# Optimization experiments

Hardware: AMD Instinct MI355X
Metric: run time of the kernel (lower is better)

The kernel has to match this reference:

```python
import jax, jax.numpy as jnp
import numpy as np

NUM_HEADS = 4
D_MODEL = 256
HEAD_DIM = D_MODEL // NUM_HEADS  # 64
B, N = 8, 2048


def _proj(x, W, b):
    # Conv1d with kernel_size=1 == pointwise linear over channel dim
    # x: [B, C_in, N], W: [C_out, C_in], b: [C_out]
    return jnp.einsum('oi,bin->bon', W, x) + b[None, :, None]


def setup_inputs() -> dict:
    key = jax.random.key(0)
    ks = jax.random.split(key, 11)
    s = 1.0 / np.sqrt(D_MODEL)
    return {
        'query': jax.random.normal(ks[0], (B, D_MODEL, N), jnp.float32),
        'key':   jax.random.normal(ks[1], (B, D_MODEL, N), jnp.float32),
        'value': jax.random.normal(ks[2], (B, D_MODEL, N), jnp.float32),
        'Wq': jax.random.normal(ks[3], (D_MODEL, D_MODEL), jnp.float32) * s,
        'bq': jax.random.normal(ks[4], (D_MODEL,), jnp.float32) * 0.01,
        'Wk': jax.random.normal(ks[5], (D_MODEL, D_MODEL), jnp.float32) * s,
        'bk': jax.random.normal(ks[6], (D_MODEL,), jnp.float32) * 0.01,
        'Wv': jax.random.normal(ks[7], (D_MODEL, D_MODEL), jnp.float32) * s,
        'bv': jax.random.normal(ks[8], (D_MODEL,), jnp.float32) * 0.01,
        'Wm': jax.random.normal(ks[9], (D_MODEL, D_MODEL), jnp.float32) * s,
        'bm': jax.random.normal(ks[10], (D_MODEL,), jnp.float32) * 0.01,
    }


def reference(query, key, value, Wq, bq, Wk, bk, Wv, bv, Wm, bm):
    b = query.shape[0]
    # project then split channels into (head_dim, num_heads): [B, d, h, N]
    q = _proj(query, Wq, bq).reshape(b, HEAD_DIM, NUM_HEADS, -1)
    k = _proj(key,   Wk, bk).reshape(b, HEAD_DIM, NUM_HEADS, -1)
    v = _proj(value, Wv, bv).reshape(b, HEAD_DIM, NUM_HEADS, -1)
    scale = 1.0 / jnp.sqrt(jnp.asarray(HEAD_DIM, q.dtype))
    scores = jnp.einsum('bdhn,bdhm->bhnm', q, k) * scale  # [B,H,N,N]
    prob = jax.nn.softmax(scores, axis=-1)
    x = jnp.einsum('bhnm,bdhm->bdhn', prob, v)  # [B,d,H,N]
    x = x.reshape(b, HEAD_DIM * NUM_HEADS, -1)  # [B, d_model, N]
    return _proj(x, Wm, bm)
```

## Files before the change

kernel.cpp:

```cpp
#include <hip/hip_runtime.h>
#include <math.h>


constexpr int BATCH  = 8;
constexpr int DMODEL = 256;
constexpr int SEQ    = 2048;
constexpr int HDIM   = 64;
constexpr int TM     = 64;
constexpr int NJT    = SEQ / TM;

typedef _Float16 half2_t __attribute__((ext_vector_type(2)));
typedef _Float16 half4_t __attribute__((ext_vector_type(4)));
typedef _Float16 half8_t __attribute__((ext_vector_type(8)));
typedef float    float4_t __attribute__((ext_vector_type(4)));

static __device__ __forceinline__ void ld16_lds(const void* g, void* l) {
    __builtin_amdgcn_global_load_lds(
        (const __attribute__((address_space(1))) unsigned*)g,
        (__attribute__((address_space(3))) unsigned*)l, 16, 0, 0);
}

static __device__ __forceinline__ half8_t cvt8(const float4 w0, const float4 w1) {
    half8_t a;
    a[0] = (_Float16)w0.x; a[1] = (_Float16)w0.y;
    a[2] = (_Float16)w0.z; a[3] = (_Float16)w0.w;
    a[4] = (_Float16)w1.x; a[5] = (_Float16)w1.y;
    a[6] = (_Float16)w1.z; a[7] = (_Float16)w1.w;
    return a;
}

__global__ __launch_bounds__(256, 3)
void gemm_qkv(const float* __restrict__ Wq, const float* __restrict__ Wk,
              const float* __restrict__ Wv, const float* __restrict__ Wm,
              const float* __restrict__ bq, const float* __restrict__ bk,
              const float* __restrict__ bv,
              const float* __restrict__ Xq, const float* __restrict__ Xk,
              const float* __restrict__ Xv, _Float16* __restrict__ qT,
              _Float16* __restrict__ kT, _Float16* __restrict__ vT,
              _Float16* __restrict__ wfp)
{
    if (blockIdx.y == 24) {
        const int r = blockIdx.x * 8 + (threadIdx.x >> 5);
        const int c32 = threadIdx.x & 31;
        half8_t o8;
        #pragma unroll
        for (int e = 0; e < 8; ++e) {
            const int hd = c32 * 8 + e;
            o8[e] = (_Float16)Wm[r * DMODEL + 4 * (hd & 63) + (hd >> 6)];
        }
        *(half8_t*)&wfp[(size_t)r * DMODEL + c32 * 8] = o8;
        return;
    }

    const int n0 = blockIdx.x * 64;
    const int proj = blockIdx.y >> 3, b = blockIdx.y & 7;
    const float* W    = proj == 0 ? Wq : proj == 1 ? Wk : Wv;
    const float* bias = proj == 0 ? bq : proj == 1 ? bk : bv;
    const float* X    = (proj == 0 ? Xq : proj == 1 ? Xk : Xv)
                        + (size_t)b * DMODEL * SEQ;
    const float qs = (proj == 0) ? 0.18033688011112042f : 1.0f;

    __shared__ __align__(16) char lds[50432];
    float*    T  = (float*)lds;
    _Float16* Xs = (_Float16*)(lds + 16640);
    _Float16* Tw = (_Float16*)lds;

    const int tid = threadIdx.x, tn = tid & 15, tc = tid >> 4;

    #pragma unroll
    for (int cc = 0; cc < 4; ++cc) {
        __syncthreads();
        #pragma unroll
        for (int i = 0; i < 4; ++i) {
            const int c = tc + 16 * i;
            const float4 v = *(const float4*)&X[(size_t)(cc * 64 + c) * SEQ + n0 + tn * 4];
            T[c * 65 + tn * 4 + 0] = v.x; T[c * 65 + tn * 4 + 1] = v.y;
            T[c * 65 + tn * 4 + 2] = v.z; T[c * 65 + tn * 4 + 3] = v.w;
        }
        __syncthreads();
        #pragma unroll
        for (int i = 0; i < 4; ++i) {
            const int n = tc + 16 * i;
            half4_t h4;
            #pragma unroll
            for (int j = 0; j < 4; ++j) h4[j] = (_Float16)T[(tn * 4 + j) * 65 + n];
            *(half4_t*)&Xs[n * 264 + cc * 64 + tn * 4] = h4;
        }
    }
    __syncthreads();

    const int w = tid >> 6, lane = tid & 63;
    const int lm = lane & 15, g = lane >> 4, g8 = g * 8;
    const int cw0 = w * 64;

    float4_t acc[4][4];
    #pragma unroll
    for (int mt = 0; mt < 4; ++mt)
        #pragma unroll
        for (int nt = 0; nt < 4; ++nt) acc[mt][nt] = (float4_t){0.f, 0.f, 0.f, 0.f};

    #pragma unroll
    for (int k0 = 0; k0 < DMODEL; k0 += 64) {
        half8_t a[4][2], bb[4][2];
        #pragma unroll
        for (int mt = 0; mt < 4; ++mt)
            #pragma unroll
            for (int kd = 0; kd < 2; ++kd) {
                const float* wp = &W[(size_t)(cw0 + mt * 16 + lm) * DMODEL
                                     + k0 + kd * 32 + g8];
                a[mt][kd] = cvt8(*(const float4*)wp, *(const float4*)(wp + 4));
            }
        #pragma unroll
        for (int nt = 0; nt < 4; ++nt)
            #pragma unroll
            for (int kd = 0; kd < 2; ++kd)
                bb[nt][kd] = *(const half8_t*)&Xs[(nt * 16 + lm) * 264
                                                  + k0 + kd * 32 + g8];
        #pragma unroll
        for (int kd = 0; kd < 2; ++kd)
            #pragma unroll
            for (int mt = 0; mt < 4; ++mt)
                #pragma unroll
                for (int nt = 0; nt < 4; ++nt)
                    acc[mt][nt] = __builtin_amdgcn_mfma_f32_16x16x32_f16(
                        a[mt][kd], bb[nt][kd], acc[mt][nt], 0, 0, 0);
    }
    __syncthreads();

    #pragma unroll
    for (int mt = 0; mt < 4; ++mt) {
        const float4 b4 = *(const float4*)&bias[cw0 + mt * 16 + g * 4];
        const float bb4[4] = {b4.x, b4.y, b4.z, b4.w};
        #pragma unroll
        for (int nt = 0; nt < 4; ++nt) {
            half4_t pk;
            #pragma unroll
            for (int r = 0; r < 4; ++r)
                pk[r] = (_Float16)((acc[mt][nt][r] + bb4[r]) * qs);
            *(half4_t*)&Tw[((w * 64 + nt * 16 + lm)) * 68 + mt * 16 + g * 4] = pk;
        }
    }
    __syncthreads();

    if (proj < 2) {
        _Float16* dst = (proj == 0 ? qT : kT);
        const int h = w;
        const int dcg = lane & 7, nlb = lane >> 3;
        #pragma unroll
        for (int it = 0; it < 8; ++it) {
            const int nl = it * 8 + nlb;
            const int hs = (nl & 3) | (((nl >> 3) & 1) << 2);
            half8_t ch;
            #pragma unroll
            for (int e = 0; e < 8; ++e) {
                ch[e] = Tw[((dcg >> 1) * 64 + nl) * 68
                           + 4 * ((dcg & 1) * 8 + e) + h];
            }
            const int chunk = dcg ^ hs;
            *(half8_t*)&dst[((size_t)(b * 4 + h) * SEQ + n0 + nl) * HDIM
                            + chunk * 8] = ch;
        }
    } else {
        const int h = w;
        const int jc = lane & 7, db = lane >> 3;
        const size_t tilebase =
            (((size_t)(b * 4 + h) * NJT + (n0 >> 6)) * HDIM) * (size_t)TM;
        #pragma unroll
        for (int it = 0; it < 8; ++it) {
            const int d = it * 8 + db;
            half8_t ch;
            #pragma unroll
            for (int e = 0; e < 8; ++e) {
                ch[e] = Tw[((d >> 4) * 64 + jc * 8 + e) * 68
                           + 4 * (d & 15) + h];
            }
            *(half8_t*)&vT[tilebase + (size_t)d * TM + ((jc ^ (d & 7)) << 3)] = ch;
        }
    }
}

__global__ __launch_bounds__(256, 2)
void attn_f16(const _Float16* __restrict__ qT, const _Float16* __restrict__ kT,
              const _Float16* __restrict__ vT, _Float16* __restrict__ xp)
{
    const int lid = blockIdx.x;
    const int work = (lid & 7) * 64 + (lid >> 3);
    const int bh = work >> 4, b = bh >> 2, h = bh & 3;
    const int ib = work & 15;
    const int tid = threadIdx.x, wid = tid >> 6, lane = tid & 63;
    const int lm = lane & 15, g = lane >> 4;
    const int i0 = ib * 128 + wid * 32;

    __shared__ _Float16 Kb[2][TM * HDIM];
    __shared__ _Float16 Vb[2][TM * HDIM];

    const int hq = (lm & 3) | (((lm >> 3) & 1) << 2);
    const int hk = (lm & 3) | (((lm >> 2) & 1) << 2);
    const int rbase = 8 * (lm >> 2) + (lm & 3);

    half8_t bq[2][2];
    const _Float16* qbase = qT + (size_t)bh * SEQ * HDIM;
    #pragma unroll
    for (int rt = 0; rt < 2; ++rt)
        #pragma unroll
        for (int kd = 0; kd < 2; ++kd) {
            const int row = i0 + rt * 16 + lm;
            bq[rt][kd] = *(const half8_t*)(qbase + (size_t)row * HDIM
                                           + (((kd * 4 + g) ^ hq) << 3));
        }

    const char* kt = (const char*)(kT + (size_t)bh * SEQ * HDIM);
    const char* vt = (const char*)(vT + (size_t)bh * NJT * TM * HDIM);

    float4_t o[2][4];
    float rsum[2][2] = {{0.f, 0.f}, {0.f, 0.f}};
    #pragma unroll
    for (int rt = 0; rt < 2; ++rt)
        #pragma unroll
        for (int dt = 0; dt < 4; ++dt) o[rt][dt] = (float4_t){0.f, 0.f, 0.f, 0.f};

    #define STAGE(jt, bu)                                                     \
        {                                                                     \
            const char* kg = kt + (size_t)(jt) * 8192;                        \
            const char* vg = vt + (size_t)(jt) * 8192;                        \
            _Pragma("unroll")                                                 \
            for (int p = 0; p < 2; ++p) {                                     \
                const int c = wid + p * 4;                                    \
                ld16_lds(kg + c * 1024 + lane * 16, (char*)&Kb[bu][0] + c * 1024); \
                ld16_lds(vg + c * 1024 + lane * 16, (char*)&Vb[bu][0] + c * 1024); \
            }                                                                 \
        }

    STAGE(0, 0);
    __syncthreads();

    for (int jt = 0; jt < NJT; ++jt) {
        const int cur = jt & 1;
        if (jt + 1 < NJT) STAGE(jt + 1, cur ^ 1);

        float4_t s[2][2][2];
        #pragma unroll
        for (int jb = 0; jb < 2; ++jb)
            #pragma unroll
            for (int u = 0; u < 2; ++u)
                #pragma unroll
                for (int rt = 0; rt < 2; ++rt)
                    s[jb][u][rt] = (float4_t){0.f, 0.f, 0.f, 0.f};
        #pragma unroll
        for (int kd = 0; kd < 2; ++kd)
            #pragma unroll
            for (int jb = 0; jb < 2; ++jb)
                #pragma unroll
                for (int u = 0; u < 2; ++u) {
                    const int jrow = jb * 32 + rbase + 4 * u;
                    const half8_t fk = *(const half8_t*)
                        &Kb[cur][jrow * HDIM + (((kd * 4 + g) ^ hk) << 3)];
                    #pragma unroll
                    for (int rt = 0; rt < 2; ++rt)
                        s[jb][u][rt] = __builtin_amdgcn_mfma_f32_16x16x32_f16(
                            fk, bq[rt][kd], s[jb][u][rt], 0, 0, 0);
                }

        half8_t ap[2][2];
        #pragma unroll
        for (int jb = 0; jb < 2; ++jb)
            #pragma unroll
            for (int rt = 0; rt < 2; ++rt) {
                half8_t p;
                #pragma unroll
                for (int r = 0; r < 4; ++r) {
                    const float e0 = __builtin_amdgcn_exp2f(s[jb][0][rt][r]);
                    const float e1 = __builtin_amdgcn_exp2f(s[jb][1][rt][r]);
                    rsum[jb][rt] += e0;
                    rsum[jb][rt] += e1;
                    p[r]     = (_Float16)e0;
                    p[r + 4] = (_Float16)e1;
                }
                ap[jb][rt] = p;
            }

        #pragma unroll
        for (int jb = 0; jb < 2; ++jb)
            #pragma unroll
            for (int dt = 0; dt < 4; ++dt) {
                const int d = dt * 16 + lm;
                const half8_t fv = *(const half8_t*)
                    &Vb[cur][d * TM + (((jb * 4 + g) ^ (lm & 7)) << 3)];
                #pragma unroll
                for (int rt = 0; rt < 2; ++rt)
                    o[rt][dt] = __builtin_amdgcn_mfma_f32_16x16x32_f16(
                        ap[jb][rt], fv, o[rt][dt], 0, 0, 0);
            }
        __syncthreads();
    }

    #pragma unroll
    for (int rt = 0; rt < 2; ++rt) {
        float v = rsum[0][rt] + rsum[1][rt];
        v += __shfl_xor(v, 16);
        v += __shfl_xor(v, 32);
        float inv[4];
        #pragma unroll
        for (int r = 0; r < 4; ++r)
            inv[r] = 1.0f / __shfl(v, 4 * g + r);
        #pragma unroll
        for (int dt = 0; dt < 4; ++dt) {
            const int d = dt * 16 + lm;
            #pragma unroll
            for (int r = 0; r < 4; ++r) {
                const int n = i0 + rt * 16 + 4 * g + r;
                xp[((size_t)b * SEQ + n) * DMODEL + h * HDIM + d] =
                    (_Float16)(o[rt][dt][r] * inv[r]);
            }
        }
    }
    #undef STAGE
}

__global__ __launch_bounds__(256, 3)
void gemm_final(const _Float16* __restrict__ wfp, const float* __restrict__ bias,
                const _Float16* __restrict__ xp, float* __restrict__ out)
{
    const int n0 = blockIdx.x * 32, b = blockIdx.y;
    const int tid = threadIdx.x, w = tid >> 6, lane = tid & 63;
    const int lm = lane & 15, g = lane >> 4, g8 = g * 8;
    const int cw0 = w * 64;

    __shared__ _Float16 Xc[32 * DMODEL];

    {
        const int c8 = tid & 31, nb = tid >> 5;
        const _Float16* P = xp + ((size_t)b * SEQ + n0) * DMODEL;
        #pragma unroll
        for (int j = 0; j < 4; ++j) {
            const int n = nb * 4 + j;
            const half8_t v = *(const half8_t*)&P[(size_t)n * DMODEL + c8 * 8];
            *(half8_t*)&Xc[n * DMODEL + ((c8 ^ (n & 7)) << 3)] = v;
        }
    }
    __syncthreads();

    float4_t acc[4][2];
    #pragma unroll
    for (int mt = 0; mt < 4; ++mt)
        #pragma unroll
        for (int nt = 0; nt < 2; ++nt) acc[mt][nt] = (float4_t){0.f, 0.f, 0.f, 0.f};

    #pragma unroll
    for (int k0 = 0; k0 < DMODEL; k0 += 64) {
        half8_t a[4][2], bb[2][2];
        #pragma unroll
        for (int mt = 0; mt < 4; ++mt)
            #pragma unroll
            for (int kd = 0; kd < 2; ++kd)
                a[mt][kd] = *(const half8_t*)&wfp[(size_t)(cw0 + mt * 16 + lm) * DMODEL
                                                  + k0 + kd * 32 + g8];
        #pragma unroll
        for (int nt = 0; nt < 2; ++nt)
            #pragma unroll
            for (int kd = 0; kd < 2; ++kd) {
                const int n = nt * 16 + lm;
                const int c8 = (k0 >> 3) + kd * 4 + g;
                bb[nt][kd] = *(const half8_t*)
                    &Xc[n * DMODEL + ((c8 ^ (n & 7)) << 3)];
            }
        #pragma unroll
        for (int kd = 0; kd < 2; ++kd)
            #pragma unroll
            for (int mt = 0; mt < 4; ++mt)
                #pragma unroll
                for (int nt = 0; nt < 2; ++nt)
                    acc[mt][nt] = __builtin_amdgcn_mfma_f32_16x16x32_f16(
                        a[mt][kd], bb[nt][kd], acc[mt][nt], 0, 0, 0);
    }

    #pragma unroll
    for (int mt = 0; mt < 4; ++mt)
        #pragma unroll
        for (int r = 0; r < 4; ++r) {
            const int co = cw0 + mt * 16 + g * 4 + r;
            const float bv_ = bias[co];
            #pragma unroll
            for (int nt = 0; nt < 2; ++nt)
                out[((size_t)b * DMODEL + co) * SEQ + n0 + nt * 16 + lm] =
                    acc[mt][nt][r] + bv_;
        }
}

extern "C" void kernel_launch(void* const* d_in, const int* in_sizes, int n_in,
                              void* d_out, int out_size, void* d_ws, size_t ws_size,
                              hipStream_t stream) {
    const float* query = (const float*)d_in[0];
    const float* key_  = (const float*)d_in[1];
    const float* value = (const float*)d_in[2];
    const float* Wq = (const float*)d_in[3];  const float* bq = (const float*)d_in[4];
    const float* Wk = (const float*)d_in[5];  const float* bk = (const float*)d_in[6];
    const float* Wv = (const float*)d_in[7];  const float* bv = (const float*)d_in[8];
    const float* Wm = (const float*)d_in[9];  const float* bm = (const float*)d_in[10];
    float* out = (float*)d_out;

    const size_t bufElems = (size_t)BATCH * DMODEL * SEQ;
    _Float16* qT = (_Float16*)d_ws;
    _Float16* kT = qT + bufElems;
    _Float16* vT = kT + bufElems;
    _Float16* xp = vT + bufElems;
    _Float16* wfp = xp + bufElems;

    gemm_qkv<<<dim3(SEQ / 64, 25), 256, 0, stream>>>(
        Wq, Wk, Wv, Wm, bq, bk, bv, query, key_, value, qT, kT, vT, wfp);
    attn_f16<<<dim3(512), 256, 0, stream>>>(qT, kT, vT, xp);
    gemm_final<<<dim3(SEQ / 32, BATCH), 256, 0, stream>>>(
        wfp, bm, xp, out);
}
```

Baseline: 178.6 us.

## Use 8 waves per attention block and split output GEMM over channel halves

The attention kernel goes from 4 waves handling 32 query rows each to 8 waves handling 16 rows each per 128-row block. Each wave now keeps half the accumulators, and the K/V staging is split across 8 waves with one load per wave. The final projection GEMM gains a grid dimension that splits the 256 output channels into two halves, doubling block count with smaller per-wave tiles and a higher occupancy hint. The aim is better latency hiding and more parallelism, at the cost of each K/V LDS tile being reused by fewer MFMAs per wave, and of the final GEMM reloading the X tile twice.

```diff
diff --git a/kernel.cpp b/kernel.cpp
--- a/kernel.cpp
+++ b/kernel.cpp
@@ -179,7 +179,7 @@
     }
 }
 
-__global__ __launch_bounds__(256, 2)
+__global__ __launch_bounds__(512, 2)
 void attn_f16(const _Float16* __restrict__ qT, const _Float16* __restrict__ kT,
               const _Float16* __restrict__ vT, _Float16* __restrict__ xp)
 {
@@ -189,7 +189,7 @@
     const int ib = work & 15;
     const int tid = threadIdx.x, wid = tid >> 6, lane = tid & 63;
     const int lm = lane & 15, g = lane >> 4;
-    const int i0 = ib * 128 + wid * 32;
+    const int i0 = ib * 128 + wid * 16;
 
     __shared__ _Float16 Kb[2][TM * HDIM];
     __shared__ _Float16 Vb[2][TM * HDIM];
@@ -198,37 +198,29 @@
     const int hk = (lm & 3) | (((lm >> 2) & 1) << 2);
     const int rbase = 8 * (lm >> 2) + (lm & 3);
 
-    half8_t bq[2][2];
+    half8_t bq[2];
     const _Float16* qbase = qT + (size_t)bh * SEQ * HDIM;
     #pragma unroll
-    for (int rt = 0; rt < 2; ++rt)
-        #pragma unroll
-        for (int kd = 0; kd < 2; ++kd) {
-            const int row = i0 + rt * 16 + lm;
-            bq[rt][kd] = *(const half8_t*)(qbase + (size_t)row * HDIM
-                                           + (((kd * 4 + g) ^ hq) << 3));
-        }
+    for (int kd = 0; kd < 2; ++kd) {
+        const int row = i0 + lm;
+        bq[kd] = *(const half8_t*)(qbase + (size_t)row * HDIM
+                                   + (((kd * 4 + g) ^ hq) << 3));
+    }
 
     const char* kt = (const char*)(kT + (size_t)bh * SEQ * HDIM);
     const char* vt = (const char*)(vT + (size_t)bh * NJT * TM * HDIM);
 
-    float4_t o[2][4];
-    float rsum[2][2] = {{0.f, 0.f}, {0.f, 0.f}};
-    #pragma unroll
-    for (int rt = 0; rt < 2; ++rt)
-        #pragma unroll
-        for (int dt = 0; dt < 4; ++dt) o[rt][dt] = (float4_t){0.f, 0.f, 0.f, 0.f};
+    float4_t o[4];
+    float rsum[2] = {0.f, 0.f};
+    #pragma unroll
+    for (int dt = 0; dt < 4; ++dt) o[dt] = (float4_t){0.f, 0.f, 0.f, 0.f};
 
     #define STAGE(jt, bu)                                                     \
         {                                                                     \
             const char* kg = kt + (size_t)(jt) * 8192;                        \
             const char* vg = vt + (size_t)(jt) * 8192;                        \
-            _Pragma("unroll")                                                 \
-            for (int p = 0; p < 2; ++p) {                                     \
-                const int c = wid + p * 4;                                    \
-                ld16_lds(kg + c * 1024 + lane * 16, (char*)&Kb[bu][0] + c * 1024); \
-                ld16_lds(vg + c * 1024 + lane * 16, (char*)&Vb[bu][0] + c * 1024); \
-            }                                                                 \
+            ld16_lds(kg + wid * 1024 + lane * 16, (char*)&Kb[bu][0] + wid * 1024); \
+            ld16_lds(vg + wid * 1024 + lane * 16, (char*)&Vb[bu][0] + wid * 1024); \
         }
 
     STAGE(0, 0);
@@ -238,14 +230,12 @@
         const int cur = jt & 1;
         if (jt + 1 < NJT) STAGE(jt + 1, cur ^ 1);
 
-        float4_t s[2][2][2];
+        float4_t s[2][2];
         #pragma unroll
         for (int jb = 0; jb < 2; ++jb)
             #pragma unroll
             for (int u = 0; u < 2; ++u)
-                #pragma unroll
-                for (int rt = 0; rt < 2; ++rt)
-                    s[jb][u][rt] = (float4_t){0.f, 0.f, 0.f, 0.f};
+                s[jb][u] = (float4_t){0.f, 0.f, 0.f, 0.f};
         #pragma unroll
         for (int kd = 0; kd < 2; ++kd)
             #pragma unroll
@@ -255,29 +245,25 @@
                     const int jrow = jb * 32 + rbase + 4 * u;
                     const half8_t fk = *(const half8_t*)
                         &Kb[cur][jrow * HDIM + (((kd * 4 + g) ^ hk) << 3)];
-                    #pragma unroll
-                    for (int rt = 0; rt < 2; ++rt)
-                        s[jb][u][rt] = __builtin_amdgcn_mfma_f32_16x16x32_f16(
-                            fk, bq[rt][kd], s[jb][u][rt], 0, 0, 0);
+                    s[jb][u] = __builtin_amdgcn_mfma_f32_16x16x32_f16(
+                        fk, bq[kd], s[jb][u], 0, 0, 0);
                 }
 
-        half8_t ap[2][2];
-        #pragma unroll
-        for (int jb = 0; jb < 2; ++jb)
-            #pragma unroll
-            for (int rt = 0; rt < 2; ++rt) {
-                half8_t p;
-                #pragma unroll
-                for (int r = 0; r < 4; ++r) {
-                    const float e0 = __builtin_amdgcn_exp2f(s[jb][0][rt][r]);
-                    const float e1 = __builtin_amdgcn_exp2f(s[jb][1][rt][r]);
-                    rsum[jb][rt] += e0;
-                    rsum[jb][rt] += e1;
-                    p[r]     = (_Float16)e0;
-                    p[r + 4] = (_Float16)e1;
-                }
-                ap[jb][rt] = p;
-            }
+        half8_t ap[2];
+        #pragma unroll
+        for (int jb = 0; jb < 2; ++jb) {
+            half8_t p;
+            #pragma unroll
+            for (int r = 0; r < 4; ++r) {
+                const float e0 = __builtin_amdgcn_exp2f(s[jb][0][r]);
+                const float e1 = __builtin_amdgcn_exp2f(s[jb][1][r]);
+                rsum[jb] += e0;
+                rsum[jb] += e1;
+                p[r]     = (_Float16)e0;
+                p[r + 4] = (_Float16)e1;
+            }
+            ap[jb] = p;
+        }
 
         #pragma unroll
         for (int jb = 0; jb < 2; ++jb)
@@ -286,17 +272,14 @@
                 const int d = dt * 16 + lm;
                 const half8_t fv = *(const half8_t*)
                     &Vb[cur][d * TM + (((jb * 4 + g) ^ (lm & 7)) << 3)];
-                #pragma unroll
-                for (int rt = 0; rt < 2; ++rt)
-                    o[rt][dt] = __builtin_amdgcn_mfma_f32_16x16x32_f16(
-                        ap[jb][rt], fv, o[rt][dt], 0, 0, 0);
+                o[dt] = __builtin_amdgcn_mfma_f32_16x16x32_f16(
+                    ap[jb], fv, o[dt], 0, 0, 0);
             }
         __syncthreads();
     }
 
-    #pragma unroll
-    for (int rt = 0; rt < 2; ++rt) {
-        float v = rsum[0][rt] + rsum[1][rt];
+    {
+        float v = rsum[0] + rsum[1];
         v += __shfl_xor(v, 16);
         v += __shfl_xor(v, 32);
         float inv[4];
@@ -308,23 +291,23 @@
             const int d = dt * 16 + lm;
             #pragma unroll
             for (int r = 0; r < 4; ++r) {
-                const int n = i0 + rt * 16 + 4 * g + r;
+                const int n = i0 + 4 * g + r;
                 xp[((size_t)b * SEQ + n) * DMODEL + h * HDIM + d] =
-                    (_Float16)(o[rt][dt][r] * inv[r]);
+                    (_Float16)(o[dt][r] * inv[r]);
             }
         }
     }
     #undef STAGE
 }
 
-__global__ __launch_bounds__(256, 3)
+__global__ __launch_bounds__(256, 4)
 void gemm_final(const _Float16* __restrict__ wfp, const float* __restrict__ bias,
                 const _Float16* __restrict__ xp, float* __restrict__ out)
 {
-    const int n0 = blockIdx.x * 32, b = blockIdx.y;
+    const int n0 = blockIdx.x * 32, m0 = blockIdx.y * 128, b = blockIdx.z;
     const int tid = threadIdx.x, w = tid >> 6, lane = tid & 63;
     const int lm = lane & 15, g = lane >> 4, g8 = g * 8;
-    const int cw0 = w * 64;
+    const int cw0 = m0 + w * 32;
 
     __shared__ _Float16 Xc[32 * DMODEL];
 
@@ -340,17 +323,17 @@
     }
     __syncthreads();
 
-    float4_t acc[4][2];
-    #pragma unroll
-    for (int mt = 0; mt < 4; ++mt)
+    float4_t acc[2][2];
+    #pragma unroll
+    for (int mt = 0; mt < 2; ++mt)
         #pragma unroll
         for (int nt = 0; nt < 2; ++nt) acc[mt][nt] = (float4_t){0.f, 0.f, 0.f, 0.f};
 
     #pragma unroll
     for (int k0 = 0; k0 < DMODEL; k0 += 64) {
-        half8_t a[4][2], bb[2][2];
-        #pragma unroll
-        for (int mt = 0; mt < 4; ++mt)
+        half8_t a[2][2], bb[2][2];
+        #pragma unroll
+        for (int mt = 0; mt < 2; ++mt)
             #pragma unroll
             for (int kd = 0; kd < 2; ++kd)
                 a[mt][kd] = *(const half8_t*)&wfp[(size_t)(cw0 + mt * 16 + lm) * DMODEL
@@ -367,7 +350,7 @@
         #pragma unroll
         for (int kd = 0; kd < 2; ++kd)
             #pragma unroll
-            for (int mt = 0; mt < 4; ++mt)
+            for (int mt = 0; mt < 2; ++mt)
                 #pragma unroll
                 for (int nt = 0; nt < 2; ++nt)
                     acc[mt][nt] = __builtin_amdgcn_mfma_f32_16x16x32_f16(
@@ -375,7 +358,7 @@
     }
 
     #pragma unroll
-    for (int mt = 0; mt < 4; ++mt)
+    for (int mt = 0; mt < 2; ++mt)
         #pragma unroll
         for (int r = 0; r < 4; ++r) {
             const int co = cw0 + mt * 16 + g * 4 + r;
@@ -408,7 +391,7 @@
 
     gemm_qkv<<<dim3(SEQ / 64, 25), 256, 0, stream>>>(
         Wq, Wk, Wv, Wm, bq, bk, bv, query, key_, value, qT, kT, vT, wfp);
-    attn_f16<<<dim3(512), 256, 0, stream>>>(qT, kT, vT, xp);
-    gemm_final<<<dim3(SEQ / 32, BATCH), 256, 0, stream>>>(
+    attn_f16<<<dim3(512), 512, 0, stream>>>(qT, kT, vT, xp);
+    gemm_final<<<dim3(SEQ / 32, 2, BATCH), 256, 0, stream>>>(
         wfp, bm, xp, out);
 }
```

New measurement: 180.9 us. Within noise of the previous version (+1.3%).

## Interleave QK, softmax and PV with sched barriers; split final GEMM over channels

Applied to the files above, without the earlier changes.

The attention inner loop is restructured so the QK product, exp and PV product run per 32-row half. Explicit sched_group_barrier directives interleave LDS reads, MFMAs and VALU exp work, and s_setprio raises wave priority during compute. The aim is to overlap exp/VALU latency with matrix-core work. Separately, the final projection GEMM is split across two output-channel halves per block, giving more blocks and higher occupancy (launch bounds 4). The cost is that the Xc tile is loaded once per half, so LDS staging is done twice. The hand-written schedule may also be fragile, and the PV macro parameter uses a non-ASCII identifier.

```diff
diff --git a/kernel.cpp b/kernel.cpp
--- a/kernel.cpp
+++ b/kernel.cpp
@@ -231,6 +231,50 @@
             }                                                                 \
         }
 
+    #define QK(jb, sdst)                                                      \
+        _Pragma("unroll")                                                     \
+        for (int kd = 0; kd < 2; ++kd)                                        \
+            _Pragma("unroll")                                                 \
+            for (int u = 0; u < 2; ++u) {                                     \
+                const int jrow = (jb) * 32 + rbase + 4 * u;                   \
+                const half8_t fk = *(const half8_t*)                          \
+                    &Kb[cur][jrow * HDIM + (((kd * 4 + g) ^ hk) << 3)];       \
+                _Pragma("unroll")                                             \
+                for (int rt = 0; rt < 2; ++rt)                                \
+                    sdst[u][rt] = __builtin_amdgcn_mfma_f32_16x16x32_f16(     \
+                        fk, bq[rt][kd], sdst[u][rt], 0, 0, 0);                \
+            }
+
+    #define EXPP(jb, ssrc, apd)                                               \
+        _Pragma("unroll")                                                     \
+        for (int rt = 0; rt < 2; ++rt) {                                      \
+            half8_t p;                                                        \
+            _Pragma("unroll")                                                 \
+            for (int r = 0; r < 4; ++r) {                                     \
+                const float e0 = __builtin_amdgcn_exp2f(ssrc[0][rt][r]);      \
+                const float e1 = __builtin_amdgcn_exp2f(ssrc[1][rt][r]);      \
+                rsum[jb][rt] += e0;                                           \
+                rsum[jb][rt] += e1;                                           \
+                p[r]     = (_Float16)e0;                                      \
+                p[r + 4] = (_Float16)e1;                                      \
+            }                                                                 \
+            apd[rt] = p;                                                      \
+        }
+
+    #define PV(jb, apس)                                                       \
+        _Pragma("unroll")                                                     \
+        for (int dt = 0; dt < 4; ++dt) {                                      \
+            const int d = dt * 16 + lm;                                       \
+            const half8_t fv = *(const half8_t*)                              \
+                &Vb[cur][d * TM + ((((jb) * 4 + g) ^ (lm & 7)) << 3)];        \
+            _Pragma("unroll")                                                 \
+            for (int rt = 0; rt < 2; ++rt)                                    \
+                o[rt][dt] = __builtin_amdgcn_mfma_f32_16x16x32_f16(           \
+                    apس[rt], fv, o[rt][dt], 0, 0, 0);                         \
+        }
+
+    #define SGB(m, n) __builtin_amdgcn_sched_group_barrier((m), (n), 0)
+
     STAGE(0, 0);
     __syncthreads();
 
@@ -238,59 +282,38 @@
         const int cur = jt & 1;
         if (jt + 1 < NJT) STAGE(jt + 1, cur ^ 1);
 
-        float4_t s[2][2][2];
-        #pragma unroll
-        for (int jb = 0; jb < 2; ++jb)
-            #pragma unroll
-            for (int u = 0; u < 2; ++u)
-                #pragma unroll
-                for (int rt = 0; rt < 2; ++rt)
-                    s[jb][u][rt] = (float4_t){0.f, 0.f, 0.f, 0.f};
-        #pragma unroll
-        for (int kd = 0; kd < 2; ++kd)
-            #pragma unroll
-            for (int jb = 0; jb < 2; ++jb)
-                #pragma unroll
-                for (int u = 0; u < 2; ++u) {
-                    const int jrow = jb * 32 + rbase + 4 * u;
-                    const half8_t fk = *(const half8_t*)
-                        &Kb[cur][jrow * HDIM + (((kd * 4 + g) ^ hk) << 3)];
-                    #pragma unroll
-                    for (int rt = 0; rt < 2; ++rt)
-                        s[jb][u][rt] = __builtin_amdgcn_mfma_f32_16x16x32_f16(
-                            fk, bq[rt][kd], s[jb][u][rt], 0, 0, 0);
-                }
-
-        half8_t ap[2][2];
-        #pragma unroll
-        for (int jb = 0; jb < 2; ++jb)
+        __builtin_amdgcn_s_setprio(1);
+
+        float4_t s0[2][2], s1[2][2];
+        #pragma unroll
+        for (int u = 0; u < 2; ++u)
             #pragma unroll
             for (int rt = 0; rt < 2; ++rt) {
-                half8_t p;
-                #pragma unroll
-                for (int r = 0; r < 4; ++r) {
-                    const float e0 = __builtin_amdgcn_exp2f(s[jb][0][rt][r]);
-                    const float e1 = __builtin_amdgcn_exp2f(s[jb][1][rt][r]);
-                    rsum[jb][rt] += e0;
-                    rsum[jb][rt] += e1;
-                    p[r]     = (_Float16)e0;
-                    p[r + 4] = (_Float16)e1;
-                }
-                ap[jb][rt] = p;
-            }
-
-        #pragma unroll
-        for (int jb = 0; jb < 2; ++jb)
-            #pragma unroll
-            for (int dt = 0; dt < 4; ++dt) {
-                const int d = dt * 16 + lm;
-                const half8_t fv = *(const half8_t*)
-                    &Vb[cur][d * TM + (((jb * 4 + g) ^ (lm & 7)) << 3)];
-                #pragma unroll
-                for (int rt = 0; rt < 2; ++rt)
-                    o[rt][dt] = __builtin_amdgcn_mfma_f32_16x16x32_f16(
-                        ap[jb][rt], fv, o[rt][dt], 0, 0, 0);
-            }
+                s0[u][rt] = (float4_t){0.f, 0.f, 0.f, 0.f};
+                s1[u][rt] = (float4_t){0.f, 0.f, 0.f, 0.f};
+            }
+
+        half8_t ap0[2], ap1[2];
+        QK(0, s0);
+        QK(1, s1);
+        EXPP(0, s0, ap0);
+        PV(0, ap0);
+        EXPP(1, s1, ap1);
+        PV(1, ap1);
+
+        SGB(0x20, 4);
+        SGB(0x100, 4); SGB(0x8, 8);
+        #pragma unroll
+        for (int i = 0; i < 4; ++i) {
+            SGB(0x100, 1); SGB(0x8, 2); SGB(0x2, 12);
+        }
+        #pragma unroll
+        for (int i = 0; i < 4; ++i) {
+            SGB(0x100, 1); SGB(0x8, 2); SGB(0x2, 12);
+        }
+        SGB(0x100, 4); SGB(0x8, 8);
+
+        __builtin_amdgcn_s_setprio(0);
         __syncthreads();
     }
 
@@ -315,16 +338,20 @@
         }
     }
     #undef STAGE
-}
-
-__global__ __launch_bounds__(256, 3)
+    #undef QK
+    #undef EXPP
+    #undef PV
+    #undef SGB
+}
+
+__global__ __launch_bounds__(256, 4)
 void gemm_final(const _Float16* __restrict__ wfp, const float* __restrict__ bias,
                 const _Float16* __restrict__ xp, float* __restrict__ out)
 {
-    const int n0 = blockIdx.x * 32, b = blockIdx.y;
+    const int n0 = blockIdx.x * 32, m0 = blockIdx.y * 128, b = blockIdx.z;
     const int tid = threadIdx.x, w = tid >> 6, lane = tid & 63;
     const int lm = lane & 15, g = lane >> 4, g8 = g * 8;
-    const int cw0 = w * 64;
+    const int cw0 = m0 + w * 32;
 
     __shared__ _Float16 Xc[32 * DMODEL];
 
@@ -340,17 +367,17 @@
     }
     __syncthreads();
 
-    float4_t acc[4][2];
-    #pragma unroll
-    for (int mt = 0; mt < 4; ++mt)
+    float4_t acc[2][2];
+    #pragma unroll
+    for (int mt = 0; mt < 2; ++mt)
         #pragma unroll
         for (int nt = 0; nt < 2; ++nt) acc[mt][nt] = (float4_t){0.f, 0.f, 0.f, 0.f};
 
     #pragma unroll
     for (int k0 = 0; k0 < DMODEL; k0 += 64) {
-        half8_t a[4][2], bb[2][2];
-        #pragma unroll
-        for (int mt = 0; mt < 4; ++mt)
+        half8_t a[2][2], bb[2][2];
+        #pragma unroll
+        for (int mt = 0; mt < 2; ++mt)
             #pragma unroll
             for (int kd = 0; kd < 2; ++kd)
                 a[mt][kd] = *(const half8_t*)&wfp[(size_t)(cw0 + mt * 16 + lm) * DMODEL
@@ -367,7 +394,7 @@
         #pragma unroll
         for (int kd = 0; kd < 2; ++kd)
             #pragma unroll
-            for (int mt = 0; mt < 4; ++mt)
+            for (int mt = 0; mt < 2; ++mt)
                 #pragma unroll
                 for (int nt = 0; nt < 2; ++nt)
                     acc[mt][nt] = __builtin_amdgcn_mfma_f32_16x16x32_f16(
@@ -375,7 +402,7 @@
     }
 
     #pragma unroll
-    for (int mt = 0; mt < 4; ++mt)
+    for (int mt = 0; mt < 2; ++mt)
         #pragma unroll
         for (int r = 0; r < 4; ++r) {
             const int co = cw0 + mt * 16 + g * 4 + r;
@@ -409,6 +436,6 @@
     gemm_qkv<<<dim3(SEQ / 64, 25), 256, 0, stream>>>(
         Wq, Wk, Wv, Wm, bq, bk, bv, query, key_, value, qT, kT, vT, wfp);
     attn_f16<<<dim3(512), 256, 0, stream>>>(qT, kT, vT, xp);
-    gemm_final<<<dim3(SEQ / 32, BATCH), 256, 0, stream>>>(
+    gemm_final<<<dim3(SEQ / 32, 2, BATCH), 256, 0, stream>>>(
         wfp, bm, xp, out);
 }
```

Result: slower. 183.7 us (+2.9%).
